# Kernel optimization log

Hardware: AMD Instinct MI355X
Metric: run time of the kernel (lower is better)

The kernel has to match this reference:

```python
import jax, jax.numpy as jnp
import numpy as np

D_MODEL = 1024
NUM_HEADS = 16
HEAD_DIM = D_MODEL // NUM_HEADS
BATCH = 2
SEQ = 2048


def setup_inputs() -> dict:
    key = jax.random.key(0)
    ks = jax.random.split(key, 9)
    s = 1.0 / np.sqrt(D_MODEL)
    X = jax.random.normal(ks[0], (BATCH, SEQ, D_MODEL), dtype=jnp.float32)
    # causal mask, broadcastable over batch and heads; masked_fill where mask == 0
    mask = jnp.tril(jnp.ones((SEQ, SEQ), dtype=jnp.int32))[None, None, :, :]
    Wq = jax.random.uniform(ks[1], (D_MODEL, D_MODEL), jnp.float32, -s, s)
    bq = jax.random.uniform(ks[2], (D_MODEL,), jnp.float32, -s, s)
    Wk = jax.random.uniform(ks[3], (D_MODEL, D_MODEL), jnp.float32, -s, s)
    bk = jax.random.uniform(ks[4], (D_MODEL,), jnp.float32, -s, s)
    Wv = jax.random.uniform(ks[5], (D_MODEL, D_MODEL), jnp.float32, -s, s)
    bv = jax.random.uniform(ks[6], (D_MODEL,), jnp.float32, -s, s)
    Wo = jax.random.uniform(ks[7], (D_MODEL, D_MODEL), jnp.float32, -s, s)
    bo = jax.random.uniform(ks[8], (D_MODEL,), jnp.float32, -s, s)
    return {"X": X, "mask": mask, "Wq": Wq, "bq": bq, "Wk": Wk, "bk": bk,
            "Wv": Wv, "bv": bv, "Wo": Wo, "bo": bo}


def reference(X, mask, Wq, bq, Wk, bk, Wv, bv, Wo, bo):
    B, S, _ = X.shape
    scale = 1.0 / np.sqrt(HEAD_DIM).astype(np.float32)

    def split_heads(t):  # [B,S,D] -> [B,H,S,Dh]
        return t.reshape(B, S, NUM_HEADS, HEAD_DIM).transpose(0, 2, 1, 3)

    q = split_heads(X @ Wq.T + bq)
    k = split_heads(X @ Wk.T + bk)
    v = split_heads(X @ Wv.T + bv)
    # [B,H,S,S] attention logits (explicitly materialized, as in the source)
    logits = jnp.einsum("bhqd,bhkd->bhqk", q, k) * scale
    logits = jnp.where(mask == 0, -jnp.inf, logits)
    attn = jax.nn.softmax(logits, axis=-1)  # dropout in eval mode: identity
    ctx = jnp.einsum("bhqk,bhkd->bhqd", attn, v)
    ctx = ctx.transpose(0, 2, 1, 3).reshape(B, S, D_MODEL)
    return ctx @ Wo.T + bo
```

## Files before the change

### kernel.cpp

```cpp
#include <hip/hip_runtime.h>


#define B_   2
#define S_   2048
#define H_   16
#define DH_  64
#define D_   1024
#define M_   (B_ * S_)

typedef __attribute__((ext_vector_type(8))) short short8;
typedef __attribute__((ext_vector_type(4))) short short4_t;
typedef float v4f __attribute__((ext_vector_type(4)));

__device__ __forceinline__ short f2bf(float f) {
    union { float f; unsigned u; } v; v.f = f;
    unsigned r = v.u + 0x7fffu + ((v.u >> 16) & 1u);
    return (short)(r >> 16);
}

#if __has_builtin(__builtin_amdgcn_exp2f)
#define EXP2(x) __builtin_amdgcn_exp2f(x)
#else
#define EXP2(x) exp2f(x)
#endif

__device__ __forceinline__ unsigned pack2(float a, float b) {
    return (__float_as_uint(a) >> 16) | (__float_as_uint(b) & 0xFFFF0000u);
}

__device__ __forceinline__ void gl2lds16(const short* g, short* l) {
    __builtin_amdgcn_global_load_lds(
        (const __attribute__((address_space(1))) unsigned int*)g,
        (__attribute__((address_space(3))) unsigned int*)l,
        16, 0, 0);
}

__global__ __launch_bounds__(256) void cast_kernel(
    const float* __restrict__ X,
    const float* __restrict__ Wq, const float* __restrict__ Wk,
    const float* __restrict__ Wv, const float* __restrict__ Wo,
    short* __restrict__ Xb, short* __restrict__ Wb)
{
    const int NX8 = (M_ * D_) / 8;
    const int NW8 = (D_ * D_) / 8;
    int idx = blockIdx.x * 256 + threadIdx.x;

    const float* src; short* dst; int off;
    if (idx < NX8) { src = X; dst = Xb; off = idx; }
    else {
        int r = idx - NX8;
        int sel = r >> 17;
        int o = r & (NW8 - 1);
        src = (sel == 0) ? Wq : (sel == 1) ? Wk : (sel == 2) ? Wv : Wo;
        dst = Wb + sel * (D_ * D_);
        off = o;
    }
    float4 f0 = ((const float4*)src)[off * 2];
    float4 f1 = ((const float4*)src)[off * 2 + 1];
    short8 s;
    s[0] = f2bf(f0.x); s[1] = f2bf(f0.y); s[2] = f2bf(f0.z); s[3] = f2bf(f0.w);
    s[4] = f2bf(f1.x); s[5] = f2bf(f1.y); s[6] = f2bf(f1.z); s[7] = f2bf(f1.w);
    *(short8*)(dst + (size_t)off * 8) = s;
}

template<int BN, int MODE>
__global__ __launch_bounds__(256) void gemm_kernel(
    const short* __restrict__ A, const short* __restrict__ W,
    const float* __restrict__ bq, const float* __restrict__ bk,
    const float* __restrict__ bv, void* __restrict__ out,
    int M, int N, int K)
{
    constexpr int SM = (MODE == 0) ? 18432 : (8192 + BN * 64);
    __shared__ __align__(16) short smem[SM];
    short* As = smem;
    short* Bs = smem + 8192;

    const int t    = threadIdx.x;
    const int lane = t & 63;
    const int wave = t >> 6;

    const int bid = blockIdx.x;
    const int by  = ((bid & 7) << 2) + ((bid >> 3) & 3);
    const int bx  = bid >> 5;
    const int m0 = by * 128;
    const int n0 = bx * BN;

    const int wm = (wave >> 1) * 64;
    const int wn = (wave & 1) * (BN / 2);
    constexpr int NJ  = BN / 32;
    constexpr int BIT = BN / 32;

    v4f acc[4][NJ] = {};

    const int rsub = lane >> 3;
    const int csw  = ((lane & 7) ^ rsub) * 8;
    const short* Ag = A + (size_t)(m0 + wave * 32 + rsub) * K + csw;
    const short* Wg = W + (size_t)(n0 + wave * (BN / 4) + rsub) * K + csw;
    short* Asw = As + (wave * 32) * 64;
    short* Bsw = Bs + (wave * (BN / 4)) * 64;

    const int lm = lane & 15;
    const int lg = lane >> 4;
    const int lm7 = lm & 7;

    for (int k0 = 0; k0 < K; k0 += 64) {
        #pragma unroll
        for (int i2 = 0; i2 < 4; ++i2)
            gl2lds16(Ag + (size_t)(i2 * 8) * K + k0, Asw + i2 * 512);
        #pragma unroll
        for (int i2 = 0; i2 < BIT; ++i2)
            gl2lds16(Wg + (size_t)(i2 * 8) * K + k0, Bsw + i2 * 512);
        __syncthreads();

        #pragma unroll
        for (int kk = 0; kk < 2; ++kk) {
            const int ch = (kk * 4 + lg) ^ lm7;
            short8 af[4], bf[NJ];
            #pragma unroll
            for (int i = 0; i < 4; ++i)
                af[i] = *(const short8*)((const char*)As + (wm + i * 16 + lm) * 128 + ch * 16);
            #pragma unroll
            for (int j = 0; j < NJ; ++j)
                bf[j] = *(const short8*)((const char*)Bs + (wn + j * 16 + lm) * 128 + ch * 16);
            #pragma unroll
            for (int i = 0; i < 4; ++i)
                #pragma unroll
                for (int j = 0; j < NJ; ++j)
                    acc[i][j] = __builtin_amdgcn_mfma_f32_16x16x32_bf16(af[i], bf[j], acc[i][j], 0, 0, 0);
        }
        __syncthreads();
    }

    const int sel = n0 >> 10;
    const float* bias = (MODE == 2) ? bq : (sel == 0) ? bq : (sel == 1) ? bk : bv;

    if constexpr (MODE == 2) {
        const int colb = n0 + wn + lm;
        const int rowb = m0 + wm + lg * 4;
        #pragma unroll
        for (int j = 0; j < NJ; ++j) {
            int col = colb + j * 16;
            float bv_ = bias[col];
            #pragma unroll
            for (int i = 0; i < 4; ++i)
                #pragma unroll
                for (int r = 0; r < 4; ++r)
                    ((float*)out)[(size_t)(rowb + i * 16 + r) * 1024 + col] = acc[i][j][r] + bv_;
        }
    } else {
        short* Es = smem + wave * (64 * 72);
        const int cb = (n0 + wn) & 1023;
        #pragma unroll
        for (int j = 0; j < 4; ++j) {
            float bv_ = bias[cb + j * 16 + lm];
            #pragma unroll
            for (int i = 0; i < 4; ++i)
                #pragma unroll
                for (int r = 0; r < 4; ++r) {
                    float vv = acc[i][j][r] + bv_;
                    if (sel == 0) vv *= 0.1803368867f;
                    if (sel < 2)
                        Es[(i * 16 + lg * 4 + r) * 72 + j * 16 + lm] = f2bf(vv);
                    else
                        Es[(j * 16 + lm) * 72 + i * 16 + lg * 4 + r] = f2bf(vv);
                }
        }
        __asm__ __volatile__("s_waitcnt lgkmcnt(0)" ::: "memory");
        short* outQKV = (short*)out;
        const int rl = lane >> 3;
        const int c8 = (lane & 7) * 8;
        const int h  = cb >> 6;
        const int b  = (m0 + wm) >> 11;
        const int bh = (b << 4) + h;
        if (sel < 2) {
            #pragma unroll
            for (int it = 0; it < 8; ++it) {
                int row_l = it * 8 + rl;
                short8 vrow = *(const short8*)&Es[row_l * 72 + c8];
                int s = (m0 + wm + row_l) & 2047;
                *(short8*)(outQKV + (size_t)sel * 4194304 +
                           ((size_t)bh * S_ + s) * DH_ + c8) = vrow;
            }
        } else {
            const int s0 = (m0 + wm) & 2047;
            #pragma unroll
            for (int it = 0; it < 8; ++it) {
                int d_l = it * 8 + rl;
                short8 vrow = *(const short8*)&Es[d_l * 72 + c8];
                *(short8*)(outQKV + (size_t)2 * 4194304 +
                           ((size_t)bh << 17) + ((size_t)d_l << 11) + s0 + c8) = vrow;
            }
        }
    }
}

__global__ __launch_bounds__(512, 2) void attn_kernel(
    const short* __restrict__ Q, const short* __restrict__ Kh,
    const short* __restrict__ Vt, short* __restrict__ ctx)
{
    __shared__ __align__(16) short sm[16384];
    short* Kt = sm;
    short* Vp = sm + 8192;

    const int t    = threadIdx.x;
    const int lane = t & 63;
    const int w    = t >> 6;
    const int bid  = blockIdx.x;

    const int lo  = bid & 255;
    const int xcd = lo & 7;
    const int idx = lo >> 3;
    const int bh  = (xcd << 2) + (idx & 3);
    const int jb  = idx >> 2;
    const int j   = (bid < 256) ? jb : (15 - jb);
    const int q0  = j * 128;
    const int npairs = j + 1;
    const int qr0 = q0 + w * 16;

    const int lm = lane & 15;
    const int lg = lane >> 4;

    const short* Qb = Q  + (size_t)bh * S_ * DH_;
    const short* Kb = Kh + (size_t)bh * S_ * DH_;
    const short* Vb = Vt + ((size_t)bh << 17);

    short8 qf[2];
    #pragma unroll
    for (int kk = 0; kk < 2; ++kk)
        qf[kk] = *(const short8*)(Qb + (size_t)(qr0 + lm) * DH_ + kk * 32 + lg * 8);

    float m_i = -1e30f, l_i = 0.f;
    v4f o[4] = {};

    for (int it = 0; it < npairs; ++it) {
        const int kv0 = it * 128;
        const bool dpair = (it == npairs - 1);

        {
            const int rsub = lane >> 3;
            const int csw  = ((lane & 7) ^ rsub) * 8;
            #pragma unroll
            for (int i2 = 0; i2 < 2; ++i2) {
                const int rb = w * 16 + i2 * 8;
                gl2lds16(Kb + (size_t)(kv0 + rb + rsub) * 64 + csw, Kt + rb * 64);
            }
        }
        {
            const int d  = w * 8 + (lane >> 3);
            const int s3 = d & 7;
            short8 vld[2];
            #pragma unroll
            for (int m = 0; m < 2; ++m) {
                const int cm = (lane & 7) + 8 * m;
                vld[m] = *(const short8*)(Vb + (size_t)d * 2048 + kv0 + cm * 8);
            }
            char* vrow = (char*)Vp + d * 256;
            #pragma unroll
            for (int m = 0; m < 2; ++m) {
                const int cm = (lane & 7) + 8 * m;
                const int u  = cm >> 3, kk = (cm >> 2) & 1;
                const int q0off = ((cm & 1) << 4) + ((cm >> 1) & 1) * 4;
                const int bA = (u * 64 + kk * 32 + q0off) * 2;
                const int pA = ((((bA >> 4) ^ s3) << 4) | (bA & 15));
                const int bB = bA + 16;
                const int pB = ((((bB >> 4) ^ s3) << 4) | (bB & 15));
                *(short4_t*)(vrow + pA) = __builtin_shufflevector(vld[m], vld[m], 0, 1, 2, 3);
                *(short4_t*)(vrow + pB) = __builtin_shufflevector(vld[m], vld[m], 4, 5, 6, 7);
            }
        }
        __syncthreads();

        short8 vf[2][2][4];
        #pragma unroll
        for (int u = 0; u < 2; ++u)
            #pragma unroll
            for (int kk = 0; kk < 2; ++kk)
                #pragma unroll
                for (int i = 0; i < 4; ++i) {
                    const int d = i * 16 + lm;
                    const int ch = (u * 8 + kk * 4 + lg) ^ (lm & 7);
                    vf[u][kk][i] = *(const short8*)((const char*)Vp + d * 256 + ch * 16);
                }

        v4f sc[2][4] = {};
        #pragma unroll
        for (int u = 0; u < 2; ++u) {
            short8 kf[2][4];
            #pragma unroll
            for (int kk = 0; kk < 2; ++kk)
                #pragma unroll
                for (int jj = 0; jj < 4; ++jj) {
                    const int row = u * 64 + jj * 16 + lm;
                    const int ch  = (kk * 4 + lg) ^ (lm & 7);
                    kf[kk][jj] = *(const short8*)((const char*)Kt + row * 128 + ch * 16);
                }
            #pragma unroll
            for (int kk = 0; kk < 2; ++kk)
                #pragma unroll
                for (int jj = 0; jj < 4; ++jj)
                    sc[u][jj] = __builtin_amdgcn_mfma_f32_16x16x32_bf16(kf[kk][jj], qf[kk], sc[u][jj], 0, 0, 0);
        }

        float alpha;
        short8 pf[2][2];
        {
            float x[2][4][4];
            const int q = qr0 + lm;
            #pragma unroll
            for (int u = 0; u < 2; ++u)
                #pragma unroll
                for (int jj = 0; jj < 4; ++jj)
                    #pragma unroll
                    for (int r = 0; r < 4; ++r) {
                        float v = sc[u][jj][r];
                        if (dpair && (kv0 + u * 64 + jj * 16 + lg * 4 + r > q)) v = -1e30f;
                        x[u][jj][r] = v;
                    }
            float m8[8];
            #pragma unroll
            for (int z = 0; z < 8; ++z) {
                const float* xz = x[z >> 2][z & 3];
                m8[z] = fmaxf(fmaxf(xz[0], xz[1]), fmaxf(xz[2], xz[3]));
            }
            float rm = fmaxf(fmaxf(fmaxf(m8[0], m8[1]), fmaxf(m8[2], m8[3])),
                             fmaxf(fmaxf(m8[4], m8[5]), fmaxf(m8[6], m8[7])));
            rm = fmaxf(rm, __shfl_xor(rm, 16, 64));
            rm = fmaxf(rm, __shfl_xor(rm, 32, 64));

            const float mn = fmaxf(m_i, rm);
            alpha = EXP2(m_i - mn);
            m_i = mn;

            float s8[8];
            #pragma unroll
            for (int z = 0; z < 8; ++z) {
                float* xz = x[z >> 2][z & 3];
                xz[0] = EXP2(xz[0] - mn); xz[1] = EXP2(xz[1] - mn);
                xz[2] = EXP2(xz[2] - mn); xz[3] = EXP2(xz[3] - mn);
                s8[z] = (xz[0] + xz[1]) + (xz[2] + xz[3]);
            }
            float rs = ((s8[0] + s8[1]) + (s8[2] + s8[3])) + ((s8[4] + s8[5]) + (s8[6] + s8[7]));
            rs += __shfl_xor(rs, 16, 64);
            rs += __shfl_xor(rs, 32, 64);
            l_i = l_i * alpha + rs;

            #pragma unroll
            for (int u = 0; u < 2; ++u)
                #pragma unroll
                for (int kk = 0; kk < 2; ++kk) {
                    union { short8 s; uint4 d; } pk;
                    pk.d.x = pack2(x[u][2 * kk][0],     x[u][2 * kk][1]);
                    pk.d.y = pack2(x[u][2 * kk][2],     x[u][2 * kk][3]);
                    pk.d.z = pack2(x[u][2 * kk + 1][0], x[u][2 * kk + 1][1]);
                    pk.d.w = pack2(x[u][2 * kk + 1][2], x[u][2 * kk + 1][3]);
                    pf[u][kk] = pk.s;
                }
        }

        #pragma unroll
        for (int i = 0; i < 4; ++i)
            o[i] *= alpha;

        #pragma unroll
        for (int u = 0; u < 2; ++u)
            #pragma unroll
            for (int kk = 0; kk < 2; ++kk)
                #pragma unroll
                for (int i = 0; i < 4; ++i)
                    o[i] = __builtin_amdgcn_mfma_f32_16x16x32_bf16(vf[u][kk][i], pf[u][kk], o[i], 0, 0, 0);

        __syncthreads();
    }

    const int b = bh >> 4, hd = bh & 15;
    {
        const float inv = 1.f / l_i;
        const size_t base = ((size_t)(b * S_ + qr0 + lm) << 10) + (hd << 6) + lg * 4;
        #pragma unroll
        for (int i = 0; i < 4; ++i) {
            short4_t s4;
            #pragma unroll
            for (int r = 0; r < 4; ++r) s4[r] = f2bf(o[i][r] * inv);
            *(short4_t*)(ctx + base + i * 16) = s4;
        }
    }
}

extern "C" void kernel_launch(void* const* d_in, const int* in_sizes, int n_in,
                              void* d_out, int out_size, void* d_ws, size_t ws_size,
                              hipStream_t stream) {
    const float* X  = (const float*)d_in[0];
    const float* Wq = (const float*)d_in[2];
    const float* bq = (const float*)d_in[3];
    const float* Wk = (const float*)d_in[4];
    const float* bk = (const float*)d_in[5];
    const float* Wv = (const float*)d_in[6];
    const float* bv = (const float*)d_in[7];
    const float* Wo = (const float*)d_in[8];
    const float* bo = (const float*)d_in[9];
    float* out = (float*)d_out;

    short* ws  = (short*)d_ws;
    short* Xb  = ws;
    short* Wb  = Xb + 4194304;
    short* Qh  = Wb + 4194304;
    short* Kb  = Qh + 4194304;
    short* Vt  = Kb + 4194304;
    short* Ctx = Vt + 4194304;

    cast_kernel<<<4096, 256, 0, stream>>>(X, Wq, Wk, Wv, Wo, Xb, Wb);

    gemm_kernel<128, 0><<<768, 256, 0, stream>>>(
        Xb, Wb, bq, bk, bv, Qh, M_, 3 * D_, D_);

    attn_kernel<<<512, 512, 0, stream>>>(Qh, Kb, Vt, Ctx);

    gemm_kernel<64, 2><<<512, 256, 0, stream>>>(
        Ctx, Wb + 3145728, bo, bo, bo, out, M_, D_, D_);
}
```

Before: 191.1 us.

## Double-buffer K/V tiles in LDS to prefetch the next block during compute

Doubles the attention kernel's shared memory to hold two K/V stages. The next tile's K goes straight to LDS asynchronously and its V goes into registers before the current tile's MFMA work starts, and V is written to LDS after compute. This removes one barrier per iteration and hides global-load latency behind compute. The cost is 64KB of LDS per block, which may limit two-blocks-per-CU occupancy, plus extra registers held for the V prefetch.

```diff
diff --git a/kernel.cpp b/kernel.cpp
--- a/kernel.cpp
+++ b/kernel.cpp
@@ -198,9 +198,7 @@
     const short* __restrict__ Q, const short* __restrict__ Kh,
     const short* __restrict__ Vt, short* __restrict__ ctx)
 {
-    __shared__ __align__(16) short sm[16384];
-    short* Kt = sm;
-    short* Vp = sm + 8192;
+    __shared__ __align__(16) short sm[32768];
 
     const int t    = threadIdx.x;
     const int lane = t & 63;
@@ -224,6 +222,41 @@
     const short* Kb = Kh + (size_t)bh * S_ * DH_;
     const short* Vb = Vt + ((size_t)bh << 17);
 
+    const int rsubK = lane >> 3;
+    const int cswK  = ((lane & 7) ^ rsubK) * 8;
+    const int dV    = w * 8 + (lane >> 3);
+    const int s3V   = dV & 7;
+
+    auto stageK = [&](int kv0, short* Kt) {
+        #pragma unroll
+        for (int i2 = 0; i2 < 2; ++i2) {
+            const int rb = w * 16 + i2 * 8;
+            gl2lds16(Kb + (size_t)(kv0 + rb + rsubK) * 64 + cswK, Kt + rb * 64);
+        }
+    };
+    auto loadV = [&](int kv0, short8* vld) {
+        #pragma unroll
+        for (int m = 0; m < 2; ++m) {
+            const int cm = (lane & 7) + 8 * m;
+            vld[m] = *(const short8*)(Vb + (size_t)dV * 2048 + kv0 + cm * 8);
+        }
+    };
+    auto writeV = [&](const short8* vld, short* Vp) {
+        char* vrow = (char*)Vp + dV * 256;
+        #pragma unroll
+        for (int m = 0; m < 2; ++m) {
+            const int cm = (lane & 7) + 8 * m;
+            const int u  = cm >> 3, kk = (cm >> 2) & 1;
+            const int q0off = ((cm & 1) << 4) + ((cm >> 1) & 1) * 4;
+            const int bA = (u * 64 + kk * 32 + q0off) * 2;
+            const int pA = ((((bA >> 4) ^ s3V) << 4) | (bA & 15));
+            const int bB = bA + 16;
+            const int pB = ((((bB >> 4) ^ s3V) << 4) | (bB & 15));
+            *(short4_t*)(vrow + pA) = __builtin_shufflevector(vld[m], vld[m], 0, 1, 2, 3);
+            *(short4_t*)(vrow + pB) = __builtin_shufflevector(vld[m], vld[m], 4, 5, 6, 7);
+        }
+    };
+
     short8 qf[2];
     #pragma unroll
     for (int kk = 0; kk < 2; ++kk)
@@ -232,43 +265,26 @@
     float m_i = -1e30f, l_i = 0.f;
     v4f o[4] = {};
 
+    short8 vpre[2];
+    stageK(0, sm);
+    loadV(0, vpre);
+    writeV(vpre, sm + 8192);
+    __syncthreads();
+
+    int cur = 0;
     for (int it = 0; it < npairs; ++it) {
         const int kv0 = it * 128;
         const bool dpair = (it == npairs - 1);
-
-        {
-            const int rsub = lane >> 3;
-            const int csw  = ((lane & 7) ^ rsub) * 8;
-            #pragma unroll
-            for (int i2 = 0; i2 < 2; ++i2) {
-                const int rb = w * 16 + i2 * 8;
-                gl2lds16(Kb + (size_t)(kv0 + rb + rsub) * 64 + csw, Kt + rb * 64);
-            }
-        }
-        {
-            const int d  = w * 8 + (lane >> 3);
-            const int s3 = d & 7;
-            short8 vld[2];
-            #pragma unroll
-            for (int m = 0; m < 2; ++m) {
-                const int cm = (lane & 7) + 8 * m;
-                vld[m] = *(const short8*)(Vb + (size_t)d * 2048 + kv0 + cm * 8);
-            }
-            char* vrow = (char*)Vp + d * 256;
-            #pragma unroll
-            for (int m = 0; m < 2; ++m) {
-                const int cm = (lane & 7) + 8 * m;
-                const int u  = cm >> 3, kk = (cm >> 2) & 1;
-                const int q0off = ((cm & 1) << 4) + ((cm >> 1) & 1) * 4;
-                const int bA = (u * 64 + kk * 32 + q0off) * 2;
-                const int pA = ((((bA >> 4) ^ s3) << 4) | (bA & 15));
-                const int bB = bA + 16;
-                const int pB = ((((bB >> 4) ^ s3) << 4) | (bB & 15));
-                *(short4_t*)(vrow + pA) = __builtin_shufflevector(vld[m], vld[m], 0, 1, 2, 3);
-                *(short4_t*)(vrow + pB) = __builtin_shufflevector(vld[m], vld[m], 4, 5, 6, 7);
-            }
-        }
-        __syncthreads();
+        const bool pre   = (it + 1 < npairs);
+        short* Kt  = sm + cur * 16384;
+        short* Vp  = Kt + 8192;
+        short* Ktn = sm + (cur ^ 1) * 16384;
+        short* Vpn = Ktn + 8192;
+
+        if (pre) {
+            stageK(kv0 + 128, Ktn);
+            loadV(kv0 + 128, vpre);
+        }
 
         short8 vf[2][2][4];
         #pragma unroll
@@ -369,7 +385,9 @@
                 for (int i = 0; i < 4; ++i)
                     o[i] = __builtin_amdgcn_mfma_f32_16x16x32_bf16(vf[u][kk][i], pf[u][kk], o[i], 0, 0, 0);
 
+        if (pre) writeV(vpre, Vpn);
         __syncthreads();
+        cur ^= 1;
     }
 
     const int b = bh >> 4, hd = bh & 15;
```

Result: no change. 188.5 us (-1.4%).
